# Optimization experiments

Measured on AMD Instinct MI355X. Metric: run time of the kernel, lower is better.

Reference implementation:

```python
import jax, jax.numpy as jnp
import numpy as np

jax.config.update("jax_enable_x64", True)

VOCAB_R_MAX = 3.0
EPS = 1e-8


def _sanitize(x):
    # torch.nan_to_num(x, nan=0.0, posinf=10000.0, neginf=-10000.0)
    return jnp.nan_to_num(x, nan=0.0, posinf=10000.0, neginf=-10000.0)


def setup_inputs() -> dict:
    key = jax.random.key(0)
    k1, k2 = jax.random.split(key, 2)
    B, L, V, n = 2, 512, 50257, 768
    hidden_states = jax.random.normal(k1, (B, L, n + 1), dtype=jnp.float32)
    # nn.Parameter(torch.randn(V, n) * 0.01) -- tangent vectors
    weight = jax.random.normal(k2, (V, n), dtype=jnp.float32) * 0.01
    # init_temp = 1/sqrt(n_embd)
    logit_scale = jnp.asarray(1.0 / np.sqrt(n), dtype=jnp.float32)
    return {"hidden_states": hidden_states, "weight": weight, "logit_scale": logit_scale}


def _exp_map_zero(v_spatial, max_tangent_norm):
    # Lorentz exp map at origin (curvature -1), tangent vector (0, v_spatial).
    # Norm is clamped to max_tangent_norm (geodesic radius ceiling).
    r = jnp.linalg.norm(v_spatial, axis=-1, keepdims=True)  # [V,1]
    rc = jnp.minimum(r, max_tangent_norm)
    dirv = v_spatial / jnp.maximum(r, EPS)
    return jnp.concatenate([jnp.cosh(rc), jnp.sinh(rc) * dirv], axis=-1)  # [V, n+1]


def _ensure_lorentz(x):
    # Project onto the hyperboloid: x0 = sqrt(1 + ||x_spatial||^2)
    sp = x[..., 1:]
    t = jnp.sqrt(1.0 + jnp.sum(sp * sp, axis=-1, keepdims=True))
    return jnp.concatenate([t, sp], axis=-1)


def reference(hidden_states, weight, logit_scale):
    x = _ensure_lorentz(_sanitize(hidden_states))          # [B,L,n+1]
    w = _sanitize(_exp_map_zero(weight, VOCAB_R_MAX))       # [V,n+1]

    x64 = x.astype(jnp.float64)
    w64 = w.astype(jnp.float64)
    # Minkowski inner product split into time/space einsums (as in source)
    time_inner = jnp.einsum('blt,vt->blv', x64[..., :1], w64[:, :1])
    space_inner = jnp.einsum('bls,vs->blv', x64[..., 1:], w64[:, 1:])
    inner = space_inner - time_inner                        # [B,L,V] fp64

    tau = jnp.clip(logit_scale, 0.01, 2.5).astype(jnp.float64)
    logits = (inner * tau).astype(hidden_states.dtype)
    return _sanitize(logits)
```

## Files before the change

kernel.cpp:

```cpp
#include <hip/hip_runtime.h>
#include <hip/hip_bf16.h>
#include <cstdint>
#include <cstddef>

typedef __attribute__((ext_vector_type(4))) float f32x4;
typedef __attribute__((ext_vector_type(8))) short bf16x8;

#define KDIM 768
#define BM 128
#define BN 128
#define BK 64

static __device__ __forceinline__ float sani(float x) {
  if (__builtin_isnan(x)) return 0.0f;
  if (__builtin_isinf(x)) return x > 0.0f ? 1.0e4f : -1.0e4f;
  return x;
}

static __device__ __forceinline__ unsigned short f2bf(float x) {
  unsigned u = __builtin_bit_cast(unsigned, x);
  unsigned r = 0x7FFFu + ((u >> 16) & 1u);
  return (unsigned short)((u + r) >> 16);
}

__global__ __launch_bounds__(256) void prep_x_kernel(
    const float* __restrict__ h, unsigned short* __restrict__ xl,
    float* __restrict__ tx) {
  const int row = blockIdx.x;
  const int t = threadIdx.x;
  const float* src = h + (size_t)row * (KDIM + 1) + 1;
  float v0 = sani(src[t]);
  float v1 = sani(src[t + 256]);
  float v2 = sani(src[t + 512]);
  float ss = v0 * v0 + v1 * v1 + v2 * v2;
#pragma unroll
  for (int off = 32; off > 0; off >>= 1) ss += __shfl_down(ss, off);
  __shared__ float red[4];
  if ((t & 63) == 0) red[t >> 6] = ss;
  __syncthreads();
  if (t == 0) {
    float total = red[0] + red[1] + red[2] + red[3];
    tx[row] = sqrtf(1.0f + total);
  }
  unsigned short* dst = xl + (size_t)row * KDIM;
  dst[t]       = f2bf(v0);
  dst[t + 256] = f2bf(v1);
  dst[t + 512] = f2bf(v2);
}

__global__ __launch_bounds__(256) void prep_w_kernel(
    const float* __restrict__ w, unsigned short* __restrict__ wl,
    float* __restrict__ cw, int V) {
  const int row = blockIdx.x;
  const int t = threadIdx.x;
  unsigned short* dst = wl + (size_t)row * KDIM;
  if (row >= V) {
    dst[t] = 0; dst[t + 256] = 0; dst[t + 512] = 0;
    if (t == 0) cw[row] = 0.0f;
    return;
  }
  const float* src = w + (size_t)row * KDIM;
  float v0 = src[t];
  float v1 = src[t + 256];
  float v2 = src[t + 512];
  float ss = v0 * v0 + v1 * v1 + v2 * v2;
#pragma unroll
  for (int off = 32; off > 0; off >>= 1) ss += __shfl_down(ss, off);
  __shared__ float red[4];
  if ((t & 63) == 0) red[t >> 6] = ss;
  __syncthreads();
  float total = red[0] + red[1] + red[2] + red[3];
  float r = sqrtf(total);
  float rc = fminf(r, 3.0f);
  float sc = sinhf(rc) / fmaxf(r, 1e-8f);
  dst[t]       = f2bf(sani(v0 * sc));
  dst[t + 256] = f2bf(sani(v1 * sc));
  dst[t + 512] = f2bf(sani(v2 * sc));
  if (t == 0) cw[row] = sani(coshf(rc));
}

#define GLD16(gp, sp)                                               \
  __builtin_amdgcn_global_load_lds(                                 \
      (const __attribute__((address_space(1))) void*)(gp),          \
      (__attribute__((address_space(3))) void*)(sp), 16, 0, 0)

__global__ __launch_bounds__(256) void gemm_kernel(
    const unsigned short* __restrict__ xl, const unsigned short* __restrict__ wl,
    const float* __restrict__ tx, const float* __restrict__ cw,
    const float* __restrict__ ls, float* __restrict__ out,
    int V, int Mtiles) {
  __shared__ unsigned short As[BM * BK];
  __shared__ unsigned short Bs[BN * BK];

  const int tid = threadIdx.x;
  const int lane = tid & 63;
  const int wid = tid >> 6;
  const int wr = wid >> 1;
  const int wc = wid & 1;
  const int bm = blockIdx.x % Mtiles;
  const int bn = blockIdx.x / Mtiles;

  const int l15 = lane & 15;
  const int lq = lane >> 4;
  const int srow = lane >> 3;
  const int scol = (lane & 7) * 8;

  f32x4 acc[4][4];
#pragma unroll
  for (int i = 0; i < 4; ++i)
#pragma unroll
    for (int j = 0; j < 4; ++j) acc[i][j] = (f32x4){0.f, 0.f, 0.f, 0.f};

  const size_t a_row0 = (size_t)bm * BM;
  const size_t b_row0 = (size_t)bn * BN;

  for (int kt = 0; kt < KDIM / BK; ++kt) {
    const int kbase = kt * BK;
#pragma unroll
    for (int c = 0; c < 4; ++c) {
      const int chunk = wid * 4 + c;
      const int row = chunk * 8 + srow;
      GLD16(xl + (a_row0 + row) * KDIM + kbase + scol, &As[chunk * 512]);
      GLD16(wl + (b_row0 + row) * KDIM + kbase + scol, &Bs[chunk * 512]);
    }
    asm volatile("s_waitcnt vmcnt(0)" ::: "memory");
    __syncthreads();
#pragma unroll
    for (int kk = 0; kk < 2; ++kk) {
      bf16x8 af[4], bfr[4];
#pragma unroll
      for (int mi = 0; mi < 4; ++mi)
        af[mi] = *(const bf16x8*)&As[(wr * 64 + mi * 16 + l15) * BK + kk * 32 + lq * 8];
#pragma unroll
      for (int ni = 0; ni < 4; ++ni)
        bfr[ni] = *(const bf16x8*)&Bs[(wc * 64 + ni * 16 + l15) * BK + kk * 32 + lq * 8];
#pragma unroll
      for (int mi = 0; mi < 4; ++mi)
#pragma unroll
        for (int ni = 0; ni < 4; ++ni)
          acc[mi][ni] = __builtin_amdgcn_mfma_f32_16x16x32_bf16(
              af[mi], bfr[ni], acc[mi][ni], 0, 0, 0);
    }
    __syncthreads();
  }

  float tau = ls[0];
  tau = fminf(fmaxf(tau, 0.01f), 2.5f);

  float cwv[4];
  int gn[4];
#pragma unroll
  for (int ni = 0; ni < 4; ++ni) {
    gn[ni] = bn * BN + wc * 64 + ni * 16 + l15;
    cwv[ni] = (gn[ni] < V) ? cw[gn[ni]] : 0.0f;
  }
#pragma unroll
  for (int mi = 0; mi < 4; ++mi) {
    const int rbase = bm * BM + wr * 64 + mi * 16 + lq * 4;
    const f32x4 t4 = *(const f32x4*)&tx[rbase];
#pragma unroll
    for (int ni = 0; ni < 4; ++ni) {
      if (gn[ni] < V) {
#pragma unroll
        for (int j = 0; j < 4; ++j) {
          out[(size_t)(rbase + j) * V + gn[ni]] =
              (acc[mi][ni][j] - t4[j] * cwv[ni]) * tau;
        }
      }
    }
  }
}

extern "C" void kernel_launch(void* const* d_in, const int* in_sizes, int n_in,
                              void* d_out, int out_size, void* d_ws, size_t ws_size,
                              hipStream_t stream) {
  const float* h = (const float*)d_in[0];
  const float* w = (const float*)d_in[1];
  const float* ls = (const float*)d_in[2];
  float* out = (float*)d_out;

  const int M = in_sizes[0] / (KDIM + 1);
  const int V = in_sizes[1] / KDIM;
  const int Vpad = (V + BN - 1) & ~(BN - 1);

  char* ws = (char*)d_ws;
  unsigned short* wl = (unsigned short*)ws;
  unsigned short* xl = (unsigned short*)(ws + (size_t)Vpad * KDIM * 2);
  float* cw = (float*)(ws + (size_t)Vpad * KDIM * 2 + (size_t)M * KDIM * 2);
  float* tx = cw + Vpad;

  prep_x_kernel<<<dim3(M), dim3(256), 0, stream>>>(h, xl, tx);
  prep_w_kernel<<<dim3(Vpad), dim3(256), 0, stream>>>(w, wl, cw, V);

  const int Mtiles = M / BM;
  gemm_kernel<<<dim3(Mtiles * (Vpad / BN)), dim3(256), 0, stream>>>(
      xl, wl, tx, cw, ls, out, V, Mtiles);
}
```

Before: 230.0 us.

## Swizzle LDS layout, transpose MFMA operands for row-contiguous stores, remap workgroups per XCD

```diff
diff --git a/kernel.cpp b/kernel.cpp
--- a/kernel.cpp
+++ b/kernel.cpp
@@ -2,6 +2,7 @@
 #include <hip/hip_bf16.h>
 #include <cstdint>
 #include <cstddef>
+#include <cstring>
 
 typedef __attribute__((ext_vector_type(4))) float f32x4;
 typedef __attribute__((ext_vector_type(8))) short bf16x8;
@@ -22,12 +23,14 @@
   unsigned r = 0x7FFFu + ((u >> 16) & 1u);
   return (unsigned short)((u + r) >> 16);
 }
+
 
 __global__ __launch_bounds__(256) void prep_x_kernel(
     const float* __restrict__ h, unsigned short* __restrict__ xl,
     float* __restrict__ tx) {
   const int row = blockIdx.x;
   const int t = threadIdx.x;
+  const int swz = (row & 7) << 3;
   const float* src = h + (size_t)row * (KDIM + 1) + 1;
   float v0 = sani(src[t]);
   float v1 = sani(src[t + 256]);
@@ -43,9 +46,9 @@
     tx[row] = sqrtf(1.0f + total);
   }
   unsigned short* dst = xl + (size_t)row * KDIM;
-  dst[t]       = f2bf(v0);
-  dst[t + 256] = f2bf(v1);
-  dst[t + 512] = f2bf(v2);
+  dst[t ^ swz]         = f2bf(v0);
+  dst[(t + 256) ^ swz] = f2bf(v1);
+  dst[(t + 512) ^ swz] = f2bf(v2);
 }
 
 __global__ __launch_bounds__(256) void prep_w_kernel(
@@ -53,6 +56,7 @@
     float* __restrict__ cw, int V) {
   const int row = blockIdx.x;
   const int t = threadIdx.x;
+  const int swz = (row & 7) << 3;
   unsigned short* dst = wl + (size_t)row * KDIM;
   if (row >= V) {
     dst[t] = 0; dst[t + 256] = 0; dst[t + 512] = 0;
@@ -73,9 +77,9 @@
   float r = sqrtf(total);
   float rc = fminf(r, 3.0f);
   float sc = sinhf(rc) / fmaxf(r, 1e-8f);
-  dst[t]       = f2bf(sani(v0 * sc));
-  dst[t + 256] = f2bf(sani(v1 * sc));
-  dst[t + 512] = f2bf(sani(v2 * sc));
+  dst[t ^ swz]         = f2bf(sani(v0 * sc));
+  dst[(t + 256) ^ swz] = f2bf(sani(v1 * sc));
+  dst[(t + 512) ^ swz] = f2bf(sani(v2 * sc));
   if (t == 0) cw[row] = sani(coshf(rc));
 }
 
@@ -88,7 +92,7 @@
     const unsigned short* __restrict__ xl, const unsigned short* __restrict__ wl,
     const float* __restrict__ tx, const float* __restrict__ cw,
     const float* __restrict__ ls, float* __restrict__ out,
-    int V, int Mtiles) {
+    int V, int Mtiles, int nwg8) {
   __shared__ unsigned short As[BM * BK];
   __shared__ unsigned short Bs[BN * BK];
 
@@ -97,13 +101,17 @@
   const int wid = tid >> 6;
   const int wr = wid >> 1;
   const int wc = wid & 1;
-  const int bm = blockIdx.x % Mtiles;
-  const int bn = blockIdx.x / Mtiles;
+
+  const int g = blockIdx.x;
+  const int L = (g & 7) * nwg8 + (g >> 3);
+  const int bm = L & (Mtiles - 1);
+  const int bn = L / Mtiles;
 
   const int l15 = lane & 15;
   const int lq = lane >> 4;
   const int srow = lane >> 3;
   const int scol = (lane & 7) * 8;
+  const int swz = (l15 & 7) << 3;
 
   f32x4 acc[4][4];
 #pragma unroll
@@ -127,19 +135,20 @@
     __syncthreads();
 #pragma unroll
     for (int kk = 0; kk < 2; ++kk) {
+      const int koff = (kk * 32 + lq * 8) ^ swz;
       bf16x8 af[4], bfr[4];
 #pragma unroll
       for (int mi = 0; mi < 4; ++mi)
-        af[mi] = *(const bf16x8*)&As[(wr * 64 + mi * 16 + l15) * BK + kk * 32 + lq * 8];
+        af[mi] = *(const bf16x8*)&As[(wr * 64 + mi * 16 + l15) * BK + koff];
 #pragma unroll
       for (int ni = 0; ni < 4; ++ni)
-        bfr[ni] = *(const bf16x8*)&Bs[(wc * 64 + ni * 16 + l15) * BK + kk * 32 + lq * 8];
+        bfr[ni] = *(const bf16x8*)&Bs[(wc * 64 + ni * 16 + l15) * BK + koff];
 #pragma unroll
       for (int mi = 0; mi < 4; ++mi)
 #pragma unroll
         for (int ni = 0; ni < 4; ++ni)
           acc[mi][ni] = __builtin_amdgcn_mfma_f32_16x16x32_bf16(
-              af[mi], bfr[ni], acc[mi][ni], 0, 0, 0);
+              bfr[ni], af[mi], acc[mi][ni], 0, 0, 0);
     }
     __syncthreads();
   }
@@ -147,25 +156,25 @@
   float tau = ls[0];
   tau = fminf(fmaxf(tau, 0.01f), 2.5f);
 
-  float cwv[4];
-  int gn[4];
-#pragma unroll
-  for (int ni = 0; ni < 4; ++ni) {
-    gn[ni] = bn * BN + wc * 64 + ni * 16 + l15;
-    cwv[ni] = (gn[ni] < V) ? cw[gn[ni]] : 0.0f;
-  }
 #pragma unroll
   for (int mi = 0; mi < 4; ++mi) {
-    const int rbase = bm * BM + wr * 64 + mi * 16 + lq * 4;
-    const f32x4 t4 = *(const f32x4*)&tx[rbase];
+    const int mg = bm * BM + wr * 64 + mi * 16 + l15;
+    const float txm = tx[mg];
+    float* orow = out + (size_t)mg * V;
 #pragma unroll
     for (int ni = 0; ni < 4; ++ni) {
-      if (gn[ni] < V) {
-#pragma unroll
-        for (int j = 0; j < 4; ++j) {
-          out[(size_t)(rbase + j) * V + gn[ni]] =
-              (acc[mi][ni][j] - t4[j] * cwv[ni]) * tau;
-        }
+      const int nb = bn * BN + wc * 64 + ni * 16 + lq * 4;
+      const f32x4 cw4 = *(const f32x4*)&cw[nb];
+      f32x4 v;
+#pragma unroll
+      for (int j = 0; j < 4; ++j)
+        v[j] = (acc[mi][ni][j] - txm * cw4[j]) * tau;
+      if (nb + 3 < V) {
+        __builtin_memcpy(&orow[nb], &v, 16);
+      } else {
+#pragma unroll
+        for (int j = 0; j < 4; ++j)
+          if (nb + j < V) orow[nb + j] = v[j];
       }
     }
   }
@@ -193,6 +202,7 @@
   prep_w_kernel<<<dim3(Vpad), dim3(256), 0, stream>>>(w, wl, cw, V);
 
   const int Mtiles = M / BM;
-  gemm_kernel<<<dim3(Mtiles * (Vpad / BN)), dim3(256), 0, stream>>>(
-      xl, wl, tx, cw, ls, out, V, Mtiles);
-}
+  const int nwg = Mtiles * (Vpad / BN);
+  gemm_kernel<<<dim3(nwg), dim3(256), 0, stream>>>(
+      xl, wl, tx, cw, ls, out, V, Mtiles, nwg / 8);
+}
```

New measurement: 190.0 us. 1.21x faster.
